# Kernel tuning notes

Hardware: AMD Instinct MI355X
Metric: run time of the kernel (lower is better)

Reference implementation:

```python
import jax, jax.numpy as jnp
import numpy as np

B, S, H = 64, 2048, 1024

def setup_inputs() -> dict:
    key = jax.random.key(0)
    k1, k2 = jax.random.split(key)
    enc_output = jax.random.normal(k1, (B, S, H), dtype=jnp.float32)
    h_n = jax.random.normal(k2, (B, H), dtype=jnp.float32)
    return {"enc_output": enc_output, "h_n": h_n}

def reference(enc_output, h_n):
    # dec_output: [B, 1, H]
    dec_output = h_n[:, None, :]
    # scores: [B, 1, S] = dec_output @ enc_output^T
    scores = jnp.einsum('bqh,bsh->bqs', dec_output, enc_output)
    attn = jax.nn.softmax(scores, axis=2)  # softmax over S
    # context: [B, 1, H] = attn @ enc_output
    context = jnp.einsum('bqs,bsh->bqh', attn, enc_output)
    # concat decoder state and attention context: [B, 1, 2H]
    return jnp.concatenate((dec_output, context), axis=2)
```

## Files before the change

kernel.cpp:

```cpp
#include <hip/hip_runtime.h>
#include <math.h>


#define BB 64
#define SS 2048
#define HH 1024
#define NCHUNK 16
#define SCHUNK (SS / NCHUNK)
#define NWAVE 4

#define WS_ML_OFF ((size_t)BB * NCHUNK * HH)

__global__ __launch_bounds__(256) void attn_partial_kernel(
    const float* __restrict__ enc, const float* __restrict__ hn,
    float* __restrict__ ws)
{
    const int blk   = blockIdx.x;
    const int b     = blk / NCHUNK;
    const int chunk = blk % NCHUNK;
    const int tid   = threadIdx.x;
    const int wave  = tid >> 6;
    const int lane  = tid & 63;

    const float4* hn4 = (const float4*)(hn + (size_t)b * HH);
    float4 h4[4];
#pragma unroll
    for (int j = 0; j < 4; ++j) h4[j] = hn4[j * 64 + lane];

    const float4* enc4 = (const float4*)(enc + (size_t)b * SS * HH);

    float m = -INFINITY;
    float l = 0.0f;
    float4 acc[4];
#pragma unroll
    for (int j = 0; j < 4; ++j) acc[j] = make_float4(0.f, 0.f, 0.f, 0.f);

    const int s0 = chunk * SCHUNK;
    for (int s = s0 + wave; s < s0 + SCHUNK; s += NWAVE) {
        const float4* row = enc4 + (size_t)s * (HH / 4);
        float4 e[4];
#pragma unroll
        for (int j = 0; j < 4; ++j) e[j] = row[j * 64 + lane];

        float d = 0.0f;
#pragma unroll
        for (int j = 0; j < 4; ++j) {
            d += e[j].x * h4[j].x + e[j].y * h4[j].y
               + e[j].z * h4[j].z + e[j].w * h4[j].w;
        }
#pragma unroll
        for (int off = 32; off > 0; off >>= 1)
            d += __shfl_xor(d, off, 64);

        const float m_new = fmaxf(m, d);
        const float scale = __expf(m - m_new);
        const float p     = __expf(d - m_new);
        l = l * scale + p;
#pragma unroll
        for (int j = 0; j < 4; ++j) {
            acc[j].x = acc[j].x * scale + p * e[j].x;
            acc[j].y = acc[j].y * scale + p * e[j].y;
            acc[j].z = acc[j].z * scale + p * e[j].z;
            acc[j].w = acc[j].w * scale + p * e[j].w;
        }
        m = m_new;
    }

    __shared__ float s_m[NWAVE];
    __shared__ float s_l[NWAVE];
    __shared__ float s_acc[NWAVE][HH];

#pragma unroll
    for (int j = 0; j < 4; ++j)
        ((float4*)s_acc[wave])[j * 64 + lane] = acc[j];
    if (lane == 0) { s_m[wave] = m; s_l[wave] = l; }
    __syncthreads();

    float M = fmaxf(fmaxf(s_m[0], s_m[1]), fmaxf(s_m[2], s_m[3]));
    float sc[NWAVE];
    float L = 0.0f;
#pragma unroll
    for (int w = 0; w < NWAVE; ++w) {
        sc[w] = __expf(s_m[w] - M);
        L += s_l[w] * sc[w];
    }

    float4 ctx = make_float4(0.f, 0.f, 0.f, 0.f);
#pragma unroll
    for (int w = 0; w < NWAVE; ++w) {
        float4 a = ((const float4*)s_acc[w])[tid];
        ctx.x += sc[w] * a.x;  ctx.y += sc[w] * a.y;
        ctx.z += sc[w] * a.z;  ctx.w += sc[w] * a.w;
    }
    ((float4*)(ws + (size_t)blk * HH))[tid] = ctx;
    if (tid == 0) {
        ws[WS_ML_OFF + (size_t)blk * 2 + 0] = M;
        ws[WS_ML_OFF + (size_t)blk * 2 + 1] = L;
    }
}

__global__ __launch_bounds__(256) void attn_final_kernel(
    const float* __restrict__ hn, const float* __restrict__ ws,
    float* __restrict__ out)
{
    const int b   = blockIdx.x;
    const int tid = threadIdx.x;
    const float* ml = ws + WS_ML_OFF + (size_t)b * NCHUNK * 2;

    float M = -INFINITY;
#pragma unroll
    for (int c = 0; c < NCHUNK; ++c) M = fmaxf(M, ml[c * 2]);

    float sc[NCHUNK];
    float T = 0.0f;
#pragma unroll
    for (int c = 0; c < NCHUNK; ++c) {
        sc[c] = __expf(ml[c * 2] - M);
        T += sc[c] * ml[c * 2 + 1];
    }
    const float invT = 1.0f / T;

    float4 ctx = make_float4(0.f, 0.f, 0.f, 0.f);
#pragma unroll
    for (int c = 0; c < NCHUNK; ++c) {
        float4 a = ((const float4*)(ws + (size_t)(b * NCHUNK + c) * HH))[tid];
        ctx.x += sc[c] * a.x;  ctx.y += sc[c] * a.y;
        ctx.z += sc[c] * a.z;  ctx.w += sc[c] * a.w;
    }
    ctx.x *= invT; ctx.y *= invT; ctx.z *= invT; ctx.w *= invT;

    const float4 dec = ((const float4*)(hn + (size_t)b * HH))[tid];
    float4* o = (float4*)(out + (size_t)b * 2 * HH);
    o[tid]                = dec;
    o[tid + (HH / 4)]     = ctx;
}

extern "C" void kernel_launch(void* const* d_in, const int* in_sizes, int n_in,
                              void* d_out, int out_size, void* d_ws, size_t ws_size,
                              hipStream_t stream) {
    const float* enc = (const float*)d_in[0];
    const float* hn  = (const float*)d_in[1];
    float* out = (float*)d_out;
    float* ws  = (float*)d_ws;

    attn_partial_kernel<<<dim3(BB * NCHUNK), dim3(256), 0, stream>>>(enc, hn, ws);
    attn_final_kernel<<<dim3(BB), dim3(256), 0, stream>>>(hn, ws, out);
}
```

Before: 676.0 us.

## Process two rows per iteration with interleaved chunk assignment and occupancy hint

Each wave now loads and reduces two encoder rows per loop iteration, which raises memory-level parallelism and shares the online-softmax rescale between the two rows. Rows are assigned to chunks in an interleaved pattern (chunk + NCHUNK*j) instead of contiguous blocks, and the kernel gets a launch_bounds minimum of 4 blocks per multiprocessor. The aim is to hide load latency on a bandwidth-bound stream of 512MB. The cost is more register pressure, plus strided row access that may hurt DRAM page locality.

```diff
diff --git a/kernel.cpp b/kernel.cpp
--- a/kernel.cpp
+++ b/kernel.cpp
@@ -6,12 +6,14 @@
 #define SS 2048
 #define HH 1024
 #define NCHUNK 16
-#define SCHUNK (SS / NCHUNK)
+#define JCOUNT (SS / NCHUNK)
 #define NWAVE 4
+#define RPI 2
+#define NITER (JCOUNT / (NWAVE * RPI))
 
 #define WS_ML_OFF ((size_t)BB * NCHUNK * HH)
 
-__global__ __launch_bounds__(256) void attn_partial_kernel(
+__global__ __launch_bounds__(256, 4) void attn_partial_kernel(
     const float* __restrict__ enc, const float* __restrict__ hn,
     float* __restrict__ ws)
 {
@@ -35,33 +37,52 @@
 #pragma unroll
     for (int j = 0; j < 4; ++j) acc[j] = make_float4(0.f, 0.f, 0.f, 0.f);
 
-    const int s0 = chunk * SCHUNK;
-    for (int s = s0 + wave; s < s0 + SCHUNK; s += NWAVE) {
-        const float4* row = enc4 + (size_t)s * (HH / 4);
-        float4 e[4];
+    for (int k = 0; k < NITER; ++k) {
+        const int jj = (k * NWAVE + wave) * RPI;
+        const float4* r0 = enc4 + (size_t)(chunk + NCHUNK * (jj + 0)) * (HH / 4);
+        const float4* r1 = enc4 + (size_t)(chunk + NCHUNK * (jj + 1)) * (HH / 4);
+
+        float4 e0[4], e1[4];
 #pragma unroll
-        for (int j = 0; j < 4; ++j) e[j] = row[j * 64 + lane];
+        for (int j = 0; j < 4; ++j) e0[j] = r0[j * 64 + lane];
+#pragma unroll
+        for (int j = 0; j < 4; ++j) e1[j] = r1[j * 64 + lane];
 
-        float d = 0.0f;
+        float d0a = 0.f, d0b = 0.f, d1a = 0.f, d1b = 0.f;
+#pragma unroll
+        for (int j = 0; j < 2; ++j) {
+            d0a += e0[j].x * h4[j].x + e0[j].y * h4[j].y
+                 + e0[j].z * h4[j].z + e0[j].w * h4[j].w;
+            d1a += e1[j].x * h4[j].x + e1[j].y * h4[j].y
+                 + e1[j].z * h4[j].z + e1[j].w * h4[j].w;
+        }
+#pragma unroll
+        for (int j = 2; j < 4; ++j) {
+            d0b += e0[j].x * h4[j].x + e0[j].y * h4[j].y
+                 + e0[j].z * h4[j].z + e0[j].w * h4[j].w;
+            d1b += e1[j].x * h4[j].x + e1[j].y * h4[j].y
+                 + e1[j].z * h4[j].z + e1[j].w * h4[j].w;
+        }
+        float d0 = d0a + d0b;
+        float d1 = d1a + d1b;
+
+#pragma unroll
+        for (int off = 32; off > 0; off >>= 1) {
+            d0 += __shfl_xor(d0, off, 64);
+            d1 += __shfl_xor(d1, off, 64);
+        }
+
+        const float m_new = fmaxf(m, fmaxf(d0, d1));
+        const float scale = __expf(m - m_new);
+        const float p0    = __expf(d0 - m_new);
+        const float p1    = __expf(d1 - m_new);
+        l = l * scale + p0 + p1;
 #pragma unroll
         for (int j = 0; j < 4; ++j) {
-            d += e[j].x * h4[j].x + e[j].y * h4[j].y
-               + e[j].z * h4[j].z + e[j].w * h4[j].w;
-        }
-#pragma unroll
-        for (int off = 32; off > 0; off >>= 1)
-            d += __shfl_xor(d, off, 64);
-
-        const float m_new = fmaxf(m, d);
-        const float scale = __expf(m - m_new);
-        const float p     = __expf(d - m_new);
-        l = l * scale + p;
-#pragma unroll
-        for (int j = 0; j < 4; ++j) {
-            acc[j].x = acc[j].x * scale + p * e[j].x;
-            acc[j].y = acc[j].y * scale + p * e[j].y;
-            acc[j].z = acc[j].z * scale + p * e[j].z;
-            acc[j].w = acc[j].w * scale + p * e[j].w;
+            acc[j].x = fmaf(acc[j].x, scale, fmaf(p0, e0[j].x, p1 * e1[j].x));
+            acc[j].y = fmaf(acc[j].y, scale, fmaf(p0, e0[j].y, p1 * e1[j].y));
+            acc[j].z = fmaf(acc[j].z, scale, fmaf(p0, e0[j].z, p1 * e1[j].z));
+            acc[j].w = fmaf(acc[j].w, scale, fmaf(p0, e0[j].w, p1 * e1[j].w));
         }
         m = m_new;
     }
@@ -131,8 +152,8 @@
 
     const float4 dec = ((const float4*)(hn + (size_t)b * HH))[tid];
     float4* o = (float4*)(out + (size_t)b * 2 * HH);
-    o[tid]                = dec;
-    o[tid + (HH / 4)]     = ctx;
+    o[tid]            = dec;
+    o[tid + (HH / 4)] = ctx;
 }
 
 extern "C" void kernel_launch(void* const* d_in, const int* in_sizes, int n_in,
```

Result: slower. 691.8 us (+2.3%).
